# Kernel optimization log

Hardware: AMD Instinct MI355X
Metric: run time of the kernel (lower is better)

Reference implementation:

```python
import jax, jax.numpy as jnp
import numpy as np

N_ATOMS = 20000
N_EDGES = 640000
ATOM_DIM = 16
BOND_DIM = 16


def setup_inputs() -> dict:
    key = jax.random.key(0)
    k1, k2, k3, k4 = jax.random.split(key, 4)
    atom_features = jax.random.normal(k1, (N_ATOMS, ATOM_DIM), dtype=jnp.float32)
    bond_features = jax.random.normal(k2, (N_EDGES, BOND_DIM), dtype=jnp.float32)
    pair_indices = jax.random.randint(k3, (N_EDGES, 2), 0, N_ATOMS, dtype=jnp.int32)
    kernel = jax.random.normal(k4, (BOND_DIM, ATOM_DIM * ATOM_DIM), dtype=jnp.float32) * 0.05
    bias = jnp.zeros((ATOM_DIM * ATOM_DIM,), dtype=jnp.float32)
    return {
        "atom_features": atom_features,
        "bond_features": bond_features,
        "pair_indices": pair_indices,
        "kernel": kernel,
        "bias": bias,
    }


def reference(atom_features, bond_features, pair_indices, kernel, bias):
    E = bond_features.shape[0]
    d = atom_features.shape[-1]
    # project bond features to per-edge [d, d] transform matrices
    bond_mats = (bond_features @ kernel + bias).reshape(E, d, d)
    # gather neighbor (source) atom features per edge
    neigh = atom_features[pair_indices[:, 1]]  # [E, d]
    # batched small matvec: [E, d, d] x [E, d] -> [E, d]
    msgs = jnp.einsum("eij,ej->ei", bond_mats, neigh)
    # scatter-sum messages to destination atoms
    aggregated = jax.ops.segment_sum(msgs, pair_indices[:, 0], num_segments=atom_features.shape[0])
    return aggregated
```

## Files before the change

### kernel.cpp

```cpp
#include <hip/hip_runtime.h>
#include <stdint.h>


constexpr int DIM  = 16;
constexpr int CAP  = 64;
constexpr int CSTR = 16;
constexpr int OFLOW_CAP = 65536;

__global__ __launch_bounds__(256) void bin_kernel(
    const int* __restrict__ pair, int* __restrict__ counts,
    int* __restrict__ oflow_cnt, int* __restrict__ oflow,
    int2* __restrict__ bins, int n_edges)
{
    int e = blockIdx.x * blockDim.x + threadIdx.x;
    if (e >= n_edges) return;
    int2 pr = ((const int2*)pair)[e];
    int r = atomicAdd(&counts[pr.x * CSTR], 1);
    if (r < CAP) {
        bins[pr.x * CAP + r] = make_int2(e, pr.y);
    } else {
        int oi = atomicAdd(oflow_cnt, 1);
        if (oi < OFLOW_CAP) oflow[oi] = e;
    }
}

__global__ __launch_bounds__(256) void atom_kernel(
    const float* __restrict__ atom, const float* __restrict__ bond,
    const float* __restrict__ kern, const float* __restrict__ bias,
    const int* __restrict__ counts, const int2* __restrict__ bins,
    float* __restrict__ out, int n_atoms)
{
    __shared__ float Kt[272 * 16];
    __shared__ float Sl[4][272];

    const int tid  = threadIdx.x;
    const int lane = tid & 63;
    const int w    = tid >> 6;

    for (int t = tid; t < 4096; t += 256) {
        float v = kern[t];
        int k = t >> 8, rem = t & 255, i = rem >> 4, j = rem & 15;
        Kt[(k * 16 + j) * 16 + i] = v;
    }
    if (tid < 256) {
        float v = bias[tid];
        int i = tid >> 4, j = tid & 15;
        Kt[(256 + j) * 16 + i] = v;
    }
    __syncthreads();

    const int  a      = blockIdx.x * 4 + w;
    const bool active = (a < n_atoms);

    const int k4 = lane >> 2;
    const int j4 = (lane & 3) * 4;

    if (active) {
        const int deg = min(counts[a * CSTR], CAP);

        int be = 0, bs = 0;
        if (lane < deg) {
            int2 b = bins[a * CAP + lane];
            be = b.x; bs = b.y;
        }

        float4 S4  = {0.f, 0.f, 0.f, 0.f};
        float4 ns4 = {0.f, 0.f, 0.f, 0.f};
#pragma unroll 4
        for (int t = 0; t < deg; ++t) {
            const int e   = __shfl(be, t, 64);
            const int src = __shfl(bs, t, 64);
            const float  bv = bond[(size_t)e * DIM + k4];
            const float4 nv = *(const float4*)(atom + (size_t)src * DIM + j4);
            S4.x = fmaf(bv, nv.x, S4.x);
            S4.y = fmaf(bv, nv.y, S4.y);
            S4.z = fmaf(bv, nv.z, S4.z);
            S4.w = fmaf(bv, nv.w, S4.w);
            if (lane < 4) {
                ns4.x += nv.x; ns4.y += nv.y; ns4.z += nv.z; ns4.w += nv.w;
            }
        }
        *(float4*)&Sl[w][k4 * 16 + j4] = S4;
        if (lane < 4) *(float4*)&Sl[w][256 + j4] = ns4;
    }
    __syncthreads();

    if (active) {
        const int i = lane & 15, p = lane >> 4;
        float acc = 0.f;
#pragma unroll 4
        for (int q = 0; q < 68; ++q) {
            const int o = p + q * 4;
            acc = fmaf(Kt[o * 16 + i], Sl[w][o], acc);
        }
        acc += __shfl_xor(acc, 16, 64);
        acc += __shfl_xor(acc, 32, 64);
        if (lane < 16) out[(size_t)a * DIM + i] = acc;
    }
}

__global__ __launch_bounds__(256) void oflow_kernel(
    const float* __restrict__ atom, const float* __restrict__ bond,
    const int*   __restrict__ pair, const float* __restrict__ kern,
    const float* __restrict__ bias,
    const int* __restrict__ oflow_cnt, const int* __restrict__ oflow,
    float* __restrict__ out, int n_edges)
{
    int n = min(*oflow_cnt, OFLOW_CAP);
    for (int idx = blockIdx.x * blockDim.x + threadIdx.x; idx < n;
         idx += gridDim.x * blockDim.x) {
        int e   = oflow[idx];
        int dst = pair[2 * e + 0];
        int src = pair[2 * e + 1];
        float neigh[DIM], bnd[DIM], acc[DIM];
        for (int q = 0; q < DIM; ++q) neigh[q] = atom[(size_t)src * DIM + q];
        for (int q = 0; q < DIM; ++q) bnd[q]   = bond[(size_t)e * DIM + q];
#pragma unroll
        for (int ii = 0; ii < DIM; ++ii) {
            float d = 0.f;
#pragma unroll
            for (int j = 0; j < DIM; ++j) d = fmaf(bias[ii * DIM + j], neigh[j], d);
            acc[ii] = d;
        }
#pragma unroll 1
        for (int k = 0; k < DIM; ++k) {
            const float bk = bnd[k];
            const float* Kr = kern + k * (DIM * DIM);
#pragma unroll
            for (int ii = 0; ii < DIM; ++ii) {
                float d = 0.f;
#pragma unroll
                for (int j = 0; j < DIM; ++j) d = fmaf(Kr[ii * DIM + j], neigh[j], d);
                acc[ii] = fmaf(bk, d, acc[ii]);
            }
        }
#pragma unroll
        for (int ii = 0; ii < DIM; ++ii)
            atomicAdd(&out[(size_t)dst * DIM + ii], acc[ii]);
    }
}

__global__ __launch_bounds__(256) void edge_atomic_kernel(
    const float* __restrict__ atom, const float* __restrict__ bond,
    const int*   __restrict__ pair, const float* __restrict__ kern,
    const float* __restrict__ bias, float* __restrict__ out, int n_edges)
{
    int e = blockIdx.x * blockDim.x + threadIdx.x;
    if (e >= n_edges) return;
    int dst = pair[2 * e + 0];
    int src = pair[2 * e + 1];
    float neigh[DIM], bnd[DIM], acc[DIM];
    for (int q = 0; q < DIM; ++q) neigh[q] = atom[(size_t)src * DIM + q];
    for (int q = 0; q < DIM; ++q) bnd[q]   = bond[(size_t)e * DIM + q];
#pragma unroll
    for (int i = 0; i < DIM; ++i) {
        float d = 0.f;
#pragma unroll
        for (int j = 0; j < DIM; ++j) d = fmaf(bias[i * DIM + j], neigh[j], d);
        acc[i] = d;
    }
#pragma unroll 1
    for (int k = 0; k < DIM; ++k) {
        const float bk = bnd[k];
        const float* Kr = kern + k * (DIM * DIM);
#pragma unroll
        for (int i = 0; i < DIM; ++i) {
            float d = 0.f;
#pragma unroll
            for (int j = 0; j < DIM; ++j) d = fmaf(Kr[i * DIM + j], neigh[j], d);
            acc[i] = fmaf(bk, d, acc[i]);
        }
    }
#pragma unroll
    for (int i = 0; i < DIM; ++i) atomicAdd(&out[(size_t)dst * DIM + i], acc[i]);
}

extern "C" void kernel_launch(void* const* d_in, const int* in_sizes, int n_in,
                              void* d_out, int out_size, void* d_ws, size_t ws_size,
                              hipStream_t stream)
{
    const float* atom = (const float*)d_in[0];
    const float* bond = (const float*)d_in[1];
    const int*   pair = (const int*)d_in[2];
    const float* kern = (const float*)d_in[3];
    const float* bias = (const float*)d_in[4];
    float*       out  = (float*)d_out;

    const int n_edges = in_sizes[1] / DIM;
    const int n_atoms = in_sizes[0] / DIM;

    size_t counts_off = 0;
    size_t ocnt_off   = counts_off + (size_t)n_atoms * CSTR * sizeof(int);
    size_t oflow_off  = ocnt_off + sizeof(int);
    size_t bins_off   = (oflow_off + (size_t)OFLOW_CAP * sizeof(int) + 7) & ~(size_t)7;
    size_t needed     = bins_off + (size_t)n_atoms * CAP * sizeof(int2);

    const int threads = 256;

    if (ws_size >= needed) {
        int*  counts    = (int*)((char*)d_ws + counts_off);
        int*  oflow_cnt = (int*)((char*)d_ws + ocnt_off);
        int*  oflow     = (int*)((char*)d_ws + oflow_off);
        int2* bins      = (int2*)((char*)d_ws + bins_off);

        hipMemsetAsync(counts, 0,
                       (size_t)n_atoms * CSTR * sizeof(int) + sizeof(int), stream);

        bin_kernel<<<(n_edges + threads - 1) / threads, threads, 0, stream>>>(
            pair, counts, oflow_cnt, oflow, bins, n_edges);

        atom_kernel<<<(n_atoms + 3) / 4, threads, 0, stream>>>(
            atom, bond, kern, bias, counts, bins, out, n_atoms);

        oflow_kernel<<<8, threads, 0, stream>>>(
            atom, bond, pair, kern, bias, oflow_cnt, oflow, out, n_edges);
    } else {
        hipMemsetAsync(out, 0, (size_t)out_size * sizeof(float), stream);
        edge_atomic_kernel<<<(n_edges + threads - 1) / threads, threads, 0, stream>>>(
            atom, bond, pair, kern, bias, out, n_edges);
    }
}
```

Before: 181.6 us.

## Pre-gather bf16-packed bond and neighbor values into per-atom bins during binning

The binning pass now reads each edge's bond row and source atom row, packs both to bf16 by truncation, and writes them into the destination atom's bin slot (64 bytes per edge). The atom pass then streams these contiguous packed entries instead of doing random gathers of bond and atom rows. This trades an extra large scattered write and reduced input precision for contiguous reads in the aggregation. It also pads the transposed kernel tile in shared memory to avoid bank conflicts and shrinks the counter stride; an index-only fallback is kept for small workspaces.

```diff
diff --git a/kernel.cpp b/kernel.cpp
--- a/kernel.cpp
+++ b/kernel.cpp
@@ -4,48 +4,69 @@
 
 constexpr int DIM  = 16;
 constexpr int CAP  = 64;
-constexpr int CSTR = 16;
+constexpr int CSTR = 4;
 constexpr int OFLOW_CAP = 65536;
 
-__global__ __launch_bounds__(256) void bin_kernel(
+__device__ __forceinline__ uint32_t pack2(float lo, float hi) {
+    return __builtin_amdgcn_perm(__float_as_uint(hi), __float_as_uint(lo), 0x07060302u);
+}
+__device__ __forceinline__ float blo(uint32_t u) { return __uint_as_float(u << 16); }
+__device__ __forceinline__ float bhi(uint32_t u) { return __uint_as_float(u & 0xFFFF0000u); }
+
+__global__ __launch_bounds__(256) void bin_val_kernel(
+    const float* __restrict__ atom, const float* __restrict__ bond,
     const int* __restrict__ pair, int* __restrict__ counts,
     int* __restrict__ oflow_cnt, int* __restrict__ oflow,
-    int2* __restrict__ bins, int n_edges)
+    uint16_t* __restrict__ bins, int n_edges)
 {
     int e = blockIdx.x * blockDim.x + threadIdx.x;
     if (e >= n_edges) return;
     int2 pr = ((const int2*)pair)[e];
+    const float4* bp = (const float4*)(bond + (size_t)e * DIM);
+    float4 b0 = bp[0], b1 = bp[1], b2 = bp[2], b3 = bp[3];
+    const float4* ap = (const float4*)(atom + (size_t)pr.y * DIM);
+    float4 n0 = ap[0], n1 = ap[1], n2 = ap[2], n3 = ap[3];
+
     int r = atomicAdd(&counts[pr.x * CSTR], 1);
     if (r < CAP) {
-        bins[pr.x * CAP + r] = make_int2(e, pr.y);
+        uint32_t* dst = (uint32_t*)(bins + ((size_t)pr.x * CAP + r) * 32);
+        uint4 w;
+        w.x = pack2(b0.x, b0.y); w.y = pack2(b0.z, b0.w);
+        w.z = pack2(b1.x, b1.y); w.w = pack2(b1.z, b1.w);
+        ((uint4*)dst)[0] = w;
+        w.x = pack2(b2.x, b2.y); w.y = pack2(b2.z, b2.w);
+        w.z = pack2(b3.x, b3.y); w.w = pack2(b3.z, b3.w);
+        ((uint4*)dst)[1] = w;
+        w.x = pack2(n0.x, n0.y); w.y = pack2(n0.z, n0.w);
+        w.z = pack2(n1.x, n1.y); w.w = pack2(n1.z, n1.w);
+        ((uint4*)dst)[2] = w;
+        w.x = pack2(n2.x, n2.y); w.y = pack2(n2.z, n2.w);
+        w.z = pack2(n3.x, n3.y); w.w = pack2(n3.z, n3.w);
+        ((uint4*)dst)[3] = w;
     } else {
         int oi = atomicAdd(oflow_cnt, 1);
         if (oi < OFLOW_CAP) oflow[oi] = e;
     }
 }
 
-__global__ __launch_bounds__(256) void atom_kernel(
-    const float* __restrict__ atom, const float* __restrict__ bond,
-    const float* __restrict__ kern, const float* __restrict__ bias,
-    const int* __restrict__ counts, const int2* __restrict__ bins,
+__global__ __launch_bounds__(256) void atom_val_kernel(
+    const uint16_t* __restrict__ bins, const float* __restrict__ kern,
+    const float* __restrict__ bias, const int* __restrict__ counts,
     float* __restrict__ out, int n_atoms)
 {
-    __shared__ float Kt[272 * 16];
+    __shared__ float Kt[272 * 17];
     __shared__ float Sl[4][272];
 
     const int tid  = threadIdx.x;
     const int lane = tid & 63;
     const int w    = tid >> 6;
 
-    for (int t = tid; t < 4096; t += 256) {
-        float v = kern[t];
-        int k = t >> 8, rem = t & 255, i = rem >> 4, j = rem & 15;
-        Kt[(k * 16 + j) * 16 + i] = v;
-    }
-    if (tid < 256) {
-        float v = bias[tid];
-        int i = tid >> 4, j = tid & 15;
-        Kt[(256 + j) * 16 + i] = v;
+    for (int d = tid; d < 272 * 16; d += 256) {
+        const int o = d >> 4, i = d & 15;
+        float v;
+        if (o < 256) v = kern[(o >> 4) * 256 + i * 16 + (o & 15)];
+        else         v = bias[i * 16 + (o - 256)];
+        Kt[o * 17 + i] = v;
     }
     __syncthreads();
 
@@ -57,28 +78,22 @@
 
     if (active) {
         const int deg = min(counts[a * CSTR], CAP);
-
-        int be = 0, bs = 0;
-        if (lane < deg) {
-            int2 b = bins[a * CAP + lane];
-            be = b.x; bs = b.y;
-        }
+        const uint16_t* base = bins + (size_t)a * CAP * 32;
 
         float4 S4  = {0.f, 0.f, 0.f, 0.f};
         float4 ns4 = {0.f, 0.f, 0.f, 0.f};
 #pragma unroll 4
         for (int t = 0; t < deg; ++t) {
-            const int e   = __shfl(be, t, 64);
-            const int src = __shfl(bs, t, 64);
-            const float  bv = bond[(size_t)e * DIM + k4];
-            const float4 nv = *(const float4*)(atom + (size_t)src * DIM + j4);
-            S4.x = fmaf(bv, nv.x, S4.x);
-            S4.y = fmaf(bv, nv.y, S4.y);
-            S4.z = fmaf(bv, nv.z, S4.z);
-            S4.w = fmaf(bv, nv.w, S4.w);
-            if (lane < 4) {
-                ns4.x += nv.x; ns4.y += nv.y; ns4.z += nv.z; ns4.w += nv.w;
-            }
+            const uint16_t* ent = base + t * 32;
+            const float bv = blo((uint32_t)ent[k4]);
+            uint2 nv = *(const uint2*)(ent + 16 + j4);
+            const float nx = blo(nv.x), ny = bhi(nv.x);
+            const float nz = blo(nv.y), nw = bhi(nv.y);
+            S4.x = fmaf(bv, nx, S4.x);
+            S4.y = fmaf(bv, ny, S4.y);
+            S4.z = fmaf(bv, nz, S4.z);
+            S4.w = fmaf(bv, nw, S4.w);
+            if (lane < 4) { ns4.x += nx; ns4.y += ny; ns4.z += nz; ns4.w += nw; }
         }
         *(float4*)&Sl[w][k4 * 16 + j4] = S4;
         if (lane < 4) *(float4*)&Sl[w][256 + j4] = ns4;
@@ -91,8 +106,71 @@
 #pragma unroll 4
         for (int q = 0; q < 68; ++q) {
             const int o = p + q * 4;
-            acc = fmaf(Kt[o * 16 + i], Sl[w][o], acc);
-        }
+            acc = fmaf(Kt[o * 17 + i], Sl[w][o], acc);
+        }
+        acc += __shfl_xor(acc, 16, 64);
+        acc += __shfl_xor(acc, 32, 64);
+        if (lane < 16) out[(size_t)a * DIM + i] = acc;
+    }
+}
+
+__global__ __launch_bounds__(256) void bin_id_kernel(
+    const int* __restrict__ pair, int* __restrict__ counts,
+    int* __restrict__ oflow_cnt, int* __restrict__ oflow,
+    int2* __restrict__ bins, int n_edges)
+{
+    int e = blockIdx.x * blockDim.x + threadIdx.x;
+    if (e >= n_edges) return;
+    int2 pr = ((const int2*)pair)[e];
+    int r = atomicAdd(&counts[pr.x * CSTR], 1);
+    if (r < CAP) bins[pr.x * CAP + r] = make_int2(e, pr.y);
+    else { int oi = atomicAdd(oflow_cnt, 1); if (oi < OFLOW_CAP) oflow[oi] = e; }
+}
+
+__global__ __launch_bounds__(256) void atom_id_kernel(
+    const float* __restrict__ atom, const float* __restrict__ bond,
+    const float* __restrict__ kern, const float* __restrict__ bias,
+    const int* __restrict__ counts, const int2* __restrict__ bins,
+    float* __restrict__ out, int n_atoms)
+{
+    __shared__ float Kt[272 * 17];
+    __shared__ float Sl[4][272];
+    const int tid = threadIdx.x, lane = tid & 63, w = tid >> 6;
+    for (int d = tid; d < 272 * 16; d += 256) {
+        const int o = d >> 4, i = d & 15;
+        float v;
+        if (o < 256) v = kern[(o >> 4) * 256 + i * 16 + (o & 15)];
+        else         v = bias[i * 16 + (o - 256)];
+        Kt[o * 17 + i] = v;
+    }
+    __syncthreads();
+    const int a = blockIdx.x * 4 + w;
+    const bool active = (a < n_atoms);
+    const int k4 = lane >> 2, j4 = (lane & 3) * 4;
+    if (active) {
+        const int deg = min(counts[a * CSTR], CAP);
+        int be = 0, bs = 0;
+        if (lane < deg) { int2 b = bins[a * CAP + lane]; be = b.x; bs = b.y; }
+        float4 S4 = {0.f,0.f,0.f,0.f}, ns4 = {0.f,0.f,0.f,0.f};
+#pragma unroll 4
+        for (int t = 0; t < deg; ++t) {
+            const int e = __shfl(be, t, 64), src = __shfl(bs, t, 64);
+            const float bv = bond[(size_t)e * DIM + k4];
+            const float4 nv = *(const float4*)(atom + (size_t)src * DIM + j4);
+            S4.x = fmaf(bv, nv.x, S4.x); S4.y = fmaf(bv, nv.y, S4.y);
+            S4.z = fmaf(bv, nv.z, S4.z); S4.w = fmaf(bv, nv.w, S4.w);
+            if (lane < 4) { ns4.x += nv.x; ns4.y += nv.y; ns4.z += nv.z; ns4.w += nv.w; }
+        }
+        *(float4*)&Sl[w][k4 * 16 + j4] = S4;
+        if (lane < 4) *(float4*)&Sl[w][256 + j4] = ns4;
+    }
+    __syncthreads();
+    if (active) {
+        const int i = lane & 15, p = lane >> 4;
+        float acc = 0.f;
+#pragma unroll 4
+        for (int q = 0; q < 68; ++q) { const int o = p + q * 4;
+            acc = fmaf(Kt[o * 17 + i], Sl[w][o], acc); }
         acc += __shfl_xor(acc, 16, 64);
         acc += __shfl_xor(acc, 32, 64);
         if (lane < 16) out[(size_t)a * DIM + i] = acc;
@@ -109,9 +187,8 @@
     int n = min(*oflow_cnt, OFLOW_CAP);
     for (int idx = blockIdx.x * blockDim.x + threadIdx.x; idx < n;
          idx += gridDim.x * blockDim.x) {
-        int e   = oflow[idx];
-        int dst = pair[2 * e + 0];
-        int src = pair[2 * e + 1];
+        int e = oflow[idx];
+        int dst = pair[2 * e + 0], src = pair[2 * e + 1];
         float neigh[DIM], bnd[DIM], acc[DIM];
         for (int q = 0; q < DIM; ++q) neigh[q] = atom[(size_t)src * DIM + q];
         for (int q = 0; q < DIM; ++q) bnd[q]   = bond[(size_t)e * DIM + q];
@@ -125,7 +202,7 @@
 #pragma unroll 1
         for (int k = 0; k < DIM; ++k) {
             const float bk = bnd[k];
-            const float* Kr = kern + k * (DIM * DIM);
+            const float* Kr = kern + k * 256;
 #pragma unroll
             for (int ii = 0; ii < DIM; ++ii) {
                 float d = 0.f;
@@ -147,8 +224,7 @@
 {
     int e = blockIdx.x * blockDim.x + threadIdx.x;
     if (e >= n_edges) return;
-    int dst = pair[2 * e + 0];
-    int src = pair[2 * e + 1];
+    int dst = pair[2 * e + 0], src = pair[2 * e + 1];
     float neigh[DIM], bnd[DIM], acc[DIM];
     for (int q = 0; q < DIM; ++q) neigh[q] = atom[(size_t)src * DIM + q];
     for (int q = 0; q < DIM; ++q) bnd[q]   = bond[(size_t)e * DIM + q];
@@ -162,7 +238,7 @@
 #pragma unroll 1
     for (int k = 0; k < DIM; ++k) {
         const float bk = bnd[k];
-        const float* Kr = kern + k * (DIM * DIM);
+        const float* Kr = kern + k * 256;
 #pragma unroll
         for (int i = 0; i < DIM; ++i) {
             float d = 0.f;
@@ -188,35 +264,43 @@
 
     const int n_edges = in_sizes[1] / DIM;
     const int n_atoms = in_sizes[0] / DIM;
+    const int threads = 256;
+    const int eblocks = (n_edges + threads - 1) / threads;
+    const int ablocks = (n_atoms + 3) / 4;
 
     size_t counts_off = 0;
-    size_t ocnt_off   = counts_off + (size_t)n_atoms * CSTR * sizeof(int);
+    size_t ocnt_off   = (size_t)n_atoms * CSTR * sizeof(int);
     size_t oflow_off  = ocnt_off + sizeof(int);
-    size_t bins_off   = (oflow_off + (size_t)OFLOW_CAP * sizeof(int) + 7) & ~(size_t)7;
-    size_t needed     = bins_off + (size_t)n_atoms * CAP * sizeof(int2);
-
-    const int threads = 256;
-
-    if (ws_size >= needed) {
-        int*  counts    = (int*)((char*)d_ws + counts_off);
-        int*  oflow_cnt = (int*)((char*)d_ws + ocnt_off);
-        int*  oflow     = (int*)((char*)d_ws + oflow_off);
-        int2* bins      = (int2*)((char*)d_ws + bins_off);
+    size_t bins_off   = (oflow_off + (size_t)OFLOW_CAP * sizeof(int) + 63) & ~(size_t)63;
+    size_t need_val   = bins_off + (size_t)n_atoms * CAP * 64;
+    size_t need_id    = bins_off + (size_t)n_atoms * CAP * sizeof(int2);
+
+    if (ws_size >= need_id) {
+        int* counts    = (int*)((char*)d_ws + counts_off);
+        int* oflow_cnt = (int*)((char*)d_ws + ocnt_off);
+        int* oflow     = (int*)((char*)d_ws + oflow_off);
 
         hipMemsetAsync(counts, 0,
                        (size_t)n_atoms * CSTR * sizeof(int) + sizeof(int), stream);
 
-        bin_kernel<<<(n_edges + threads - 1) / threads, threads, 0, stream>>>(
-            pair, counts, oflow_cnt, oflow, bins, n_edges);
-
-        atom_kernel<<<(n_atoms + 3) / 4, threads, 0, stream>>>(
-            atom, bond, kern, bias, counts, bins, out, n_atoms);
-
+        if (ws_size >= need_val) {
+            uint16_t* bins = (uint16_t*)((char*)d_ws + bins_off);
+            bin_val_kernel<<<eblocks, threads, 0, stream>>>(
+                atom, bond, pair, counts, oflow_cnt, oflow, bins, n_edges);
+            atom_val_kernel<<<ablocks, threads, 0, stream>>>(
+                bins, kern, bias, counts, out, n_atoms);
+        } else {
+            int2* bins = (int2*)((char*)d_ws + bins_off);
+            bin_id_kernel<<<eblocks, threads, 0, stream>>>(
+                pair, counts, oflow_cnt, oflow, bins, n_edges);
+            atom_id_kernel<<<ablocks, threads, 0, stream>>>(
+                atom, bond, kern, bias, counts, bins, out, n_atoms);
+        }
         oflow_kernel<<<8, threads, 0, stream>>>(
             atom, bond, pair, kern, bias, oflow_cnt, oflow, out, n_edges);
     } else {
         hipMemsetAsync(out, 0, (size_t)out_size * sizeof(float), stream);
-        edge_atomic_kernel<<<(n_edges + threads - 1) / threads, threads, 0, stream>>>(
+        edge_atomic_kernel<<<eblocks, threads, 0, stream>>>(
             atom, bond, pair, kern, bias, out, n_edges);
     }
 }
```

After: 206.4 us. 13.7% more time.

## Stage per-edge bond and neighbor rows in LDS and drop block-wide kernel staging

Applied to the files above, without the earlier changes.

In the per-atom kernel, each lane now gathers one incident edge's full bond row and source-atom row with vectorized loads. It writes them transposed into a padded per-wave shared-memory buffer, so the accumulation loop reads LDS instead of issuing a dependent global gather per edge. The block-wide transposed copy of the kernel and bias into shared memory and its barriers are removed. The final projection reads kern and bias directly from global memory through the cache. This aims to expose memory-level parallelism for the random gathers, at the cost of more LDS per block and possibly lower occupancy.

```diff
diff --git a/kernel.cpp b/kernel.cpp
--- a/kernel.cpp
+++ b/kernel.cpp
@@ -7,7 +7,7 @@
 constexpr int CSTR = 16;
 constexpr int OFLOW_CAP = 65536;
 
-__global__ __launch_bounds__(256) void bin_kernel(
+__global__ __launch_bounds__(256) void bin_id_kernel(
     const int* __restrict__ pair, int* __restrict__ counts,
     int* __restrict__ oflow_cnt, int* __restrict__ oflow,
     int2* __restrict__ bins, int n_edges)
@@ -16,12 +16,8 @@
     if (e >= n_edges) return;
     int2 pr = ((const int2*)pair)[e];
     int r = atomicAdd(&counts[pr.x * CSTR], 1);
-    if (r < CAP) {
-        bins[pr.x * CAP + r] = make_int2(e, pr.y);
-    } else {
-        int oi = atomicAdd(oflow_cnt, 1);
-        if (oi < OFLOW_CAP) oflow[oi] = e;
-    }
+    if (r < CAP) bins[pr.x * CAP + r] = make_int2(e, pr.y);
+    else { int oi = atomicAdd(oflow_cnt, 1); if (oi < OFLOW_CAP) oflow[oi] = e; }
 }
 
 __global__ __launch_bounds__(256) void atom_kernel(
@@ -30,73 +26,79 @@
     const int* __restrict__ counts, const int2* __restrict__ bins,
     float* __restrict__ out, int n_atoms)
 {
-    __shared__ float Kt[272 * 16];
-    __shared__ float Sl[4][272];
-
-    const int tid  = threadIdx.x;
-    const int lane = tid & 63;
-    const int w    = tid >> 6;
-
-    for (int t = tid; t < 4096; t += 256) {
-        float v = kern[t];
-        int k = t >> 8, rem = t & 255, i = rem >> 4, j = rem & 15;
-        Kt[(k * 16 + j) * 16 + i] = v;
-    }
-    if (tid < 256) {
-        float v = bias[tid];
-        int i = tid >> 4, j = tid & 15;
-        Kt[(256 + j) * 16 + i] = v;
-    }
-    __syncthreads();
-
-    const int  a      = blockIdx.x * 4 + w;
-    const bool active = (a < n_atoms);
+    __shared__ float ebuf_all[4][32 * 65];
+    __shared__ float Sl_all[4][272];
+
+    const int lane = threadIdx.x & 63;
+    const int w    = threadIdx.x >> 6;
+    const int a    = blockIdx.x * 4 + w;
+    if (a >= n_atoms) return;
+
+    float* ebuf = ebuf_all[w];
+    float* Sl   = Sl_all[w];
+
+    const int deg = min(counts[a * CSTR], CAP);
+
+    if (lane < deg) {
+        int2 ent = bins[a * CAP + lane];
+        const float4* bp = (const float4*)(bond + (size_t)ent.x * DIM);
+        const float4* ap = (const float4*)(atom + (size_t)ent.y * DIM);
+        float4 b0 = bp[0], b1 = bp[1], b2 = bp[2], b3 = bp[3];
+        float4 n0 = ap[0], n1 = ap[1], n2 = ap[2], n3 = ap[3];
+        ebuf[ 0 * 65 + lane] = b0.x; ebuf[ 1 * 65 + lane] = b0.y;
+        ebuf[ 2 * 65 + lane] = b0.z; ebuf[ 3 * 65 + lane] = b0.w;
+        ebuf[ 4 * 65 + lane] = b1.x; ebuf[ 5 * 65 + lane] = b1.y;
+        ebuf[ 6 * 65 + lane] = b1.z; ebuf[ 7 * 65 + lane] = b1.w;
+        ebuf[ 8 * 65 + lane] = b2.x; ebuf[ 9 * 65 + lane] = b2.y;
+        ebuf[10 * 65 + lane] = b2.z; ebuf[11 * 65 + lane] = b2.w;
+        ebuf[12 * 65 + lane] = b3.x; ebuf[13 * 65 + lane] = b3.y;
+        ebuf[14 * 65 + lane] = b3.z; ebuf[15 * 65 + lane] = b3.w;
+        ebuf[16 * 65 + lane] = n0.x; ebuf[17 * 65 + lane] = n0.y;
+        ebuf[18 * 65 + lane] = n0.z; ebuf[19 * 65 + lane] = n0.w;
+        ebuf[20 * 65 + lane] = n1.x; ebuf[21 * 65 + lane] = n1.y;
+        ebuf[22 * 65 + lane] = n1.z; ebuf[23 * 65 + lane] = n1.w;
+        ebuf[24 * 65 + lane] = n2.x; ebuf[25 * 65 + lane] = n2.y;
+        ebuf[26 * 65 + lane] = n2.z; ebuf[27 * 65 + lane] = n2.w;
+        ebuf[28 * 65 + lane] = n3.x; ebuf[29 * 65 + lane] = n3.y;
+        ebuf[30 * 65 + lane] = n3.z; ebuf[31 * 65 + lane] = n3.w;
+    }
 
     const int k4 = lane >> 2;
     const int j4 = (lane & 3) * 4;
-
-    if (active) {
-        const int deg = min(counts[a * CSTR], CAP);
-
-        int be = 0, bs = 0;
-        if (lane < deg) {
-            int2 b = bins[a * CAP + lane];
-            be = b.x; bs = b.y;
-        }
-
-        float4 S4  = {0.f, 0.f, 0.f, 0.f};
-        float4 ns4 = {0.f, 0.f, 0.f, 0.f};
+    float4 S4  = {0.f, 0.f, 0.f, 0.f};
+    float4 ns4 = {0.f, 0.f, 0.f, 0.f};
 #pragma unroll 4
-        for (int t = 0; t < deg; ++t) {
-            const int e   = __shfl(be, t, 64);
-            const int src = __shfl(bs, t, 64);
-            const float  bv = bond[(size_t)e * DIM + k4];
-            const float4 nv = *(const float4*)(atom + (size_t)src * DIM + j4);
-            S4.x = fmaf(bv, nv.x, S4.x);
-            S4.y = fmaf(bv, nv.y, S4.y);
-            S4.z = fmaf(bv, nv.z, S4.z);
-            S4.w = fmaf(bv, nv.w, S4.w);
-            if (lane < 4) {
-                ns4.x += nv.x; ns4.y += nv.y; ns4.z += nv.z; ns4.w += nv.w;
-            }
-        }
-        *(float4*)&Sl[w][k4 * 16 + j4] = S4;
-        if (lane < 4) *(float4*)&Sl[w][256 + j4] = ns4;
-    }
-    __syncthreads();
-
-    if (active) {
-        const int i = lane & 15, p = lane >> 4;
-        float acc = 0.f;
-#pragma unroll 4
-        for (int q = 0; q < 68; ++q) {
-            const int o = p + q * 4;
-            acc = fmaf(Kt[o * 16 + i], Sl[w][o], acc);
-        }
-        acc += __shfl_xor(acc, 16, 64);
-        acc += __shfl_xor(acc, 32, 64);
-        if (lane < 16) out[(size_t)a * DIM + i] = acc;
-    }
+    for (int t = 0; t < deg; ++t) {
+        const float bv = ebuf[k4 * 65 + t];
+        const float nx = ebuf[(16 + j4 + 0) * 65 + t];
+        const float ny = ebuf[(16 + j4 + 1) * 65 + t];
+        const float nz = ebuf[(16 + j4 + 2) * 65 + t];
+        const float nw = ebuf[(16 + j4 + 3) * 65 + t];
+        S4.x = fmaf(bv, nx, S4.x);
+        S4.y = fmaf(bv, ny, S4.y);
+        S4.z = fmaf(bv, nz, S4.z);
+        S4.w = fmaf(bv, nw, S4.w);
+        if (lane < 4) { ns4.x += nx; ns4.y += ny; ns4.z += nz; ns4.w += nw; }
+    }
+    *(float4*)&Sl[k4 * 16 + j4] = S4;
+    if (lane < 4) *(float4*)&Sl[256 + j4] = ns4;
+
+    const int i = lane & 15, p = lane >> 4;
+    float acc = 0.f;
+#pragma unroll 8
+    for (int q = 0; q < 64; ++q) {
+        const int o = p + q * 4;
+        const int k = o >> 4, j = o & 15;
+        acc = fmaf(kern[k * 256 + i * 16 + j], Sl[o], acc);
+    }
+#pragma unroll
+    for (int q2 = 0; q2 < 4; ++q2) {
+        const int jb = p + q2 * 4;
+        acc = fmaf(bias[i * 16 + jb], Sl[256 + jb], acc);
+    }
+    acc += __shfl_xor(acc, 16, 64);
+    acc += __shfl_xor(acc, 32, 64);
+    if (lane < 16) out[(size_t)a * DIM + i] = acc;
 }
 
 __global__ __launch_bounds__(256) void oflow_kernel(
@@ -109,9 +111,8 @@
     int n = min(*oflow_cnt, OFLOW_CAP);
     for (int idx = blockIdx.x * blockDim.x + threadIdx.x; idx < n;
          idx += gridDim.x * blockDim.x) {
-        int e   = oflow[idx];
-        int dst = pair[2 * e + 0];
-        int src = pair[2 * e + 1];
+        int e = oflow[idx];
+        int dst = pair[2 * e + 0], src = pair[2 * e + 1];
         float neigh[DIM], bnd[DIM], acc[DIM];
         for (int q = 0; q < DIM; ++q) neigh[q] = atom[(size_t)src * DIM + q];
         for (int q = 0; q < DIM; ++q) bnd[q]   = bond[(size_t)e * DIM + q];
@@ -125,7 +126,7 @@
 #pragma unroll 1
         for (int k = 0; k < DIM; ++k) {
             const float bk = bnd[k];
-            const float* Kr = kern + k * (DIM * DIM);
+            const float* Kr = kern + k * 256;
 #pragma unroll
             for (int ii = 0; ii < DIM; ++ii) {
                 float d = 0.f;
@@ -147,8 +148,7 @@
 {
     int e = blockIdx.x * blockDim.x + threadIdx.x;
     if (e >= n_edges) return;
-    int dst = pair[2 * e + 0];
-    int src = pair[2 * e + 1];
+    int dst = pair[2 * e + 0], src = pair[2 * e + 1];
     float neigh[DIM], bnd[DIM], acc[DIM];
     for (int q = 0; q < DIM; ++q) neigh[q] = atom[(size_t)src * DIM + q];
     for (int q = 0; q < DIM; ++q) bnd[q]   = bond[(size_t)e * DIM + q];
@@ -162,7 +162,7 @@
 #pragma unroll 1
     for (int k = 0; k < DIM; ++k) {
         const float bk = bnd[k];
-        const float* Kr = kern + k * (DIM * DIM);
+        const float* Kr = kern + k * 256;
 #pragma unroll
         for (int i = 0; i < DIM; ++i) {
             float d = 0.f;
@@ -188,14 +188,15 @@
 
     const int n_edges = in_sizes[1] / DIM;
     const int n_atoms = in_sizes[0] / DIM;
+    const int threads = 256;
+    const int eblocks = (n_edges + threads - 1) / threads;
+    const int ablocks = (n_atoms + 3) / 4;
 
     size_t counts_off = 0;
-    size_t ocnt_off   = counts_off + (size_t)n_atoms * CSTR * sizeof(int);
+    size_t ocnt_off   = (size_t)n_atoms * CSTR * sizeof(int);
     size_t oflow_off  = ocnt_off + sizeof(int);
-    size_t bins_off   = (oflow_off + (size_t)OFLOW_CAP * sizeof(int) + 7) & ~(size_t)7;
+    size_t bins_off   = (oflow_off + (size_t)OFLOW_CAP * sizeof(int) + 63) & ~(size_t)63;
     size_t needed     = bins_off + (size_t)n_atoms * CAP * sizeof(int2);
-
-    const int threads = 256;
 
     if (ws_size >= needed) {
         int*  counts    = (int*)((char*)d_ws + counts_off);
@@ -206,17 +207,17 @@
         hipMemsetAsync(counts, 0,
                        (size_t)n_atoms * CSTR * sizeof(int) + sizeof(int), stream);
 
-        bin_kernel<<<(n_edges + threads - 1) / threads, threads, 0, stream>>>(
+        bin_id_kernel<<<eblocks, threads, 0, stream>>>(
             pair, counts, oflow_cnt, oflow, bins, n_edges);
 
-        atom_kernel<<<(n_atoms + 3) / 4, threads, 0, stream>>>(
+        atom_kernel<<<ablocks, threads, 0, stream>>>(
             atom, bond, kern, bias, counts, bins, out, n_atoms);
 
         oflow_kernel<<<8, threads, 0, stream>>>(
             atom, bond, pair, kern, bias, oflow_cnt, oflow, out, n_edges);
     } else {
         hipMemsetAsync(out, 0, (size_t)out_size * sizeof(float), stream);
-        edge_atomic_kernel<<<(n_edges + threads - 1) / threads, threads, 0, stream>>>(
+        edge_atomic_kernel<<<eblocks, threads, 0, stream>>>(
             atom, bond, pair, kern, bias, out, n_edges);
     }
 }
```

Result: slower. 280.6 us (+54.6%).
